# Kernel optimization log

Measured on AMD Instinct MI355X. Metric: run time of the kernel, lower is better.

## Reference

```python
import jax, jax.numpy as jnp
import numpy as np

BSZ, L, D = 8, 2048, 1024

def setup_inputs() -> dict:
    key = jax.random.key(0)
    k1, k2, k3, k4 = jax.random.split(key, 4)
    s = 1.0 / np.sqrt(D)
    return {
        "x":   jax.random.normal(k1, (BSZ, L, D), dtype=jnp.float32),
        "A":   jax.random.normal(k2, (D,), dtype=jnp.float32),
        "W_B": jax.random.normal(k3, (D, D), dtype=jnp.float32) * s,
        "b_B": jnp.zeros((D,), dtype=jnp.float32),
        "W_C": jax.random.normal(k4, (D, D), dtype=jnp.float32) * s,
        "b_C": jnp.zeros((D,), dtype=jnp.float32),
    }

def reference(x, A, W_B, b_B, W_C, b_C):
    # Precompute B(x_t) for all t in one GEMM: [B, L, D]
    Bx = jnp.einsum("bld,ed->ble", x, W_B) + b_B
    h0 = jnp.zeros((x.shape[0], x.shape[2]), dtype=x.dtype)

    def step(h, bx_t):
        h = jnp.tanh(A * h + bx_t)   # elementwise recurrence
        return h, h

    # scan over time: Bx -> [L, B, D]
    _, hs = jax.lax.scan(step, h0, jnp.swapaxes(Bx, 0, 1))
    # y_t = C(h_t), batched over all t: hs [L, B, D]
    y = jnp.einsum("lbd,ed->lbe", hs, W_C) + b_C
    return jnp.swapaxes(y, 0, 1)  # [B, L, D]
```

## Files before the change

### kernel.cpp

```cpp
#include <hip/hip_runtime.h>
#include <hip/hip_bf16.h>
#include <stdint.h>


using half8 = __attribute__((ext_vector_type(8))) _Float16;
using f32x4 = __attribute__((ext_vector_type(4))) float;

#define DEV __device__ __forceinline__

#if __has_builtin(__builtin_amdgcn_exp2f)
DEV float pexp(float x) { return __builtin_amdgcn_exp2f(x); }
constexpr float BX_SCALE = 2.8853900817779268f;
#else
DEV float pexp(float x) { return __expf(x); }
constexpr float BX_SCALE = 2.0f;
#endif

DEV ushort f2h(float x) {
  union { _Float16 f; ushort u; } c;
  c.f = (_Float16)x;
  return c.u;
}
DEV float h2f(ushort u) {
  union { ushort u; _Float16 f; } c;
  c.u = u;
  return (float)c.f;
}

DEV void gload_lds16(const void* g, void* l) {
  __builtin_amdgcn_global_load_lds((const __attribute__((address_space(1))) void*)g,
                                   (__attribute__((address_space(3))) void*)l,
                                   16, 0, 0);
}

__global__ void k_split_convert(const float* __restrict__ in, ushort* __restrict__ hi,
                                ushort* __restrict__ lo, int n4) {
  const int stride = gridDim.x * blockDim.x;
  for (int i = blockIdx.x * blockDim.x + threadIdx.x; i < n4; i += stride) {
    float4 v = reinterpret_cast<const float4*>(in)[i];
    ushort4 hv, lv;
    hv.x = f2h(v.x); lv.x = f2h(v.x - h2f(hv.x));
    hv.y = f2h(v.y); lv.y = f2h(v.y - h2f(hv.y));
    hv.z = f2h(v.z); lv.z = f2h(v.z - h2f(hv.z));
    hv.w = f2h(v.w); lv.w = f2h(v.w - h2f(hv.w));
    reinterpret_cast<ushort4*>(hi)[i] = hv;
    reinterpret_cast<ushort4*>(lo)[i] = lv;
  }
}

__global__ void k_convert(const float* __restrict__ in, ushort* __restrict__ out, int n4) {
  const int stride = gridDim.x * blockDim.x;
  for (int i = blockIdx.x * blockDim.x + threadIdx.x; i < n4; i += stride) {
    float4 v = reinterpret_cast<const float4*>(in)[i];
    ushort4 hv;
    hv.x = f2h(v.x); hv.y = f2h(v.y);
    hv.z = f2h(v.z); hv.w = f2h(v.w);
    reinterpret_cast<ushort4*>(out)[i] = hv;
  }
}

template <int SPLIT, int SCALE>
__global__ __launch_bounds__(256, 2)
void k_gemm_bt(const ushort* __restrict__ Ah, const ushort* __restrict__ Al,
               const ushort* __restrict__ Bh, const ushort* __restrict__ Bl,
               const float* __restrict__ bias, float* __restrict__ C,
               int M, int N, int K) {
  constexpr int NMAT = SPLIT ? 4 : 2;
  __shared__ __align__(1024) ushort lds[NMAT * 128 * 64];
  ushort* sAh = lds;
  ushort* sAl = lds + (SPLIT ? 8192 : 0);
  ushort* sBh = lds + (SPLIT ? 16384 : 8192);
  ushort* sBl = lds + (SPLIT ? 24576 : 8192);

  const int t = threadIdx.x;
  const int lane = t & 63;
  const int w = t >> 6;
  const int wm = w >> 1, wn = w & 1;

  int bm, bn;
  if (gridDim.x == 8) {
    const int l = blockIdx.y * 8 + blockIdx.x;
    const int xcd = l & 7, s = l >> 3;
    bm = ((s >> 3) << 3) | xcd;
    bn = s & 7;
  } else {
    bm = blockIdx.y; bn = blockIdx.x;
  }

  const int lr = lane & 15;
  const int lk = (lane >> 4) << 3;

  const ushort* gA_h = Ah + (size_t)(bm * 128) * K;
  const ushort* gA_l = SPLIT ? (Al + (size_t)(bm * 128) * K) : gA_h;
  const ushort* gB_h = Bh + (size_t)(bn * 128) * K;
  const ushort* gB_l = SPLIT ? (Bl + (size_t)(bn * 128) * K) : gB_h;

  f32x4 acc[4][4];
#pragma unroll
  for (int i = 0; i < 4; ++i)
#pragma unroll
    for (int j = 0; j < 4; ++j)
#pragma unroll
      for (int r = 0; r < 4; ++r) acc[i][j][r] = 0.f;

  auto stage = [&](int kt) {
    const int k0 = kt * 64;
#pragma unroll
    for (int i = 0; i < 4; ++i) {
      const int lin16 = i * 256 + t;
      const int lb = lin16 << 4;
      const int row = lb >> 7;
      const int srcb = (lb & 127) ^ ((row & 7) << 4);
      const size_t goff = (size_t)row * K + (size_t)(k0 + (srcb >> 1));
      const int lidx = i * 2048 + w * 512;
      gload_lds16(gA_h + goff, sAh + lidx);
      if (SPLIT) gload_lds16(gA_l + goff, sAl + lidx);
      gload_lds16(gB_h + goff, sBh + lidx);
      if (SPLIT) gload_lds16(gB_l + goff, sBl + lidx);
    }
  };

  auto ldfrag = [&](const ushort* s, int row, int kc) -> half8 {
    const int byte = (row << 7) + (((kc << 1) ^ ((row & 7) << 4)));
    return *reinterpret_cast<const half8*>(reinterpret_cast<const char*>(s) + byte);
  };

  const int NT = K / 64;
  stage(0);
  for (int kt = 0; kt < NT; ++kt) {
    __syncthreads();
#pragma unroll
    for (int kk = 0; kk < 2; ++kk) {
      half8 ah[4], bh[4], al[4], bl[4];
      const int kc = kk * 32 + lk;
#pragma unroll
      for (int i = 0; i < 4; ++i) {
        const int row = wm * 64 + i * 16 + lr;
        ah[i] = ldfrag(sAh, row, kc);
        if (SPLIT) al[i] = ldfrag(sAl, row, kc);
      }
#pragma unroll
      for (int j = 0; j < 4; ++j) {
        const int row = wn * 64 + j * 16 + lr;
        bh[j] = ldfrag(sBh, row, kc);
        if (SPLIT) bl[j] = ldfrag(sBl, row, kc);
      }
#pragma unroll
      for (int i = 0; i < 4; ++i)
#pragma unroll
        for (int j = 0; j < 4; ++j) {
          acc[i][j] = __builtin_amdgcn_mfma_f32_16x16x32_f16(ah[i], bh[j], acc[i][j], 0, 0, 0);
          if (SPLIT) {
            acc[i][j] = __builtin_amdgcn_mfma_f32_16x16x32_f16(al[i], bh[j], acc[i][j], 0, 0, 0);
            acc[i][j] = __builtin_amdgcn_mfma_f32_16x16x32_f16(ah[i], bl[j], acc[i][j], 0, 0, 0);
          }
        }
    }
    __syncthreads();
    if (kt + 1 < NT) stage(kt + 1);
  }

  float* Cb = C + (size_t)(bm * 128) * N + bn * 128;
#pragma unroll
  for (int i = 0; i < 4; ++i)
#pragma unroll
    for (int j = 0; j < 4; ++j) {
      const int col = wn * 64 + j * 16 + lr;
      const float bv = bias[bn * 128 + col];
#pragma unroll
      for (int r = 0; r < 4; ++r) {
        const int rowt = wm * 64 + i * 16 + ((lane >> 4) << 2) + r;
        float o = acc[i][j][r] + bv;
        if (SCALE) o *= BX_SCALE;
        Cb[(size_t)rowt * N + col] = o;
      }
    }
}

__global__ __launch_bounds__(64)
void k_recurrence(const float* __restrict__ Bx2, const float* __restrict__ Avec,
                  ushort* __restrict__ Hout) {
  const int tid = blockIdx.x * 64 + threadIdx.x;
  const int b = tid >> 10;
  const int d = tid & 1023;
  const float a2 = BX_SCALE * Avec[d];
  const float* bx = Bx2 + (size_t)b * 2048 * 1024 + d;
  ushort* ho = Hout + (size_t)b * 2048 * 1024 + d;

  constexpr int P = 32;
  constexpr int NC = 2048 / P;
  float bufA[P], bufB[P];
#pragma unroll
  for (int i = 0; i < P; ++i) bufA[i] = bx[(size_t)i * 1024];
#pragma unroll
  for (int i = 0; i < P; ++i) bufB[i] = bx[(size_t)(P + i) * 1024];

  float h = 0.f;
  for (int c = 0; c < NC; c += 2) {
#pragma unroll
    for (int i = 0; i < P; ++i) {
      const float u2 = fmaf(a2, h, bufA[i]);
      const float p  = pexp(u2);
      const float r  = __builtin_amdgcn_rcpf(p + 1.f);
      h = fmaf(-2.f, r, 1.f);
      ho[(size_t)(c * P + i) * 1024] = f2h(h);
    }
    if (c + 2 < NC) {
#pragma unroll
      for (int i = 0; i < P; ++i) bufA[i] = bx[(size_t)((c + 2) * P + i) * 1024];
    }
#pragma unroll
    for (int i = 0; i < P; ++i) {
      const float u2 = fmaf(a2, h, bufB[i]);
      const float p  = pexp(u2);
      const float r  = __builtin_amdgcn_rcpf(p + 1.f);
      h = fmaf(-2.f, r, 1.f);
      ho[(size_t)((c + 1) * P + i) * 1024] = f2h(h);
    }
    if (c + 3 < NC) {
#pragma unroll
      for (int i = 0; i < P; ++i) bufB[i] = bx[(size_t)((c + 3) * P + i) * 1024];
    }
  }
}

extern "C" void kernel_launch(void* const* d_in, const int* in_sizes, int n_in,
                              void* d_out, int out_size, void* d_ws, size_t ws_size,
                              hipStream_t stream) {
  const float* x   = (const float*)d_in[0];
  const float* A   = (const float*)d_in[1];
  const float* W_B = (const float*)d_in[2];
  const float* b_B = (const float*)d_in[3];
  const float* W_C = (const float*)d_in[4];
  const float* b_C = (const float*)d_in[5];
  float* y = (float*)d_out;

  const int Bsz = 8, L = 2048, D = 1024;
  const int M = Bsz * L;

  char* ws = (char*)d_ws;
  ushort* x_hi  = (ushort*)(ws);
  ushort* x_lo  = (ushort*)(ws + 33554432);
  ushort* wb_hi = (ushort*)(ws + 67108864);
  ushort* wb_lo = (ushort*)(ws + 69206016);
  ushort* wc    = (ushort*)(ws + 71303168);
  float*  Bx    = (float*)(ws + 73400320);
  ushort* h     = x_hi;

  k_split_convert<<<2048, 256, 0, stream>>>(x, x_hi, x_lo, M * D / 4);
  k_split_convert<<<512, 256, 0, stream>>>(W_B, wb_hi, wb_lo, D * D / 4);
  k_convert<<<512, 256, 0, stream>>>(W_C, wc, D * D / 4);

  k_gemm_bt<1, 1><<<dim3(D / 128, M / 128), 256, 0, stream>>>(
      x_hi, x_lo, wb_hi, wb_lo, b_B, Bx, M, D, D);

  k_recurrence<<<(Bsz * D) / 64, 64, 0, stream>>>(Bx, A, h);

  k_gemm_bt<0, 0><<<dim3(D / 128, M / 128), 256, 0, stream>>>(
      h, (const ushort*)nullptr, wc, (const ushort*)nullptr, b_C, y, M, D, D);
}
```

Before: 232.6 us.

## Double-buffer GEMM LDS with BK=32, fuse weight conversions, simplify recurrence math

The GEMM now uses two LDS buffers with a 32-wide K step and a new swizzle. It prefetches two stages ahead and waits with explicit vmcnt counts, so global-to-LDS loads overlap MFMA work. It also raises launch bounds to allow more occupancy for the non-split GEMM. The two weight-conversion kernels are merged into one launch, and the tanh recurrence is rewritten in terms of the sigmoid reciprocal, which removes one FMA from the serial dependency chain. The hand-tuned waitcnt values and the new swizzle risk subtle hazards or bank conflicts.

```diff
diff --git a/kernel.cpp b/kernel.cpp
--- a/kernel.cpp
+++ b/kernel.cpp
@@ -48,29 +48,39 @@
   }
 }
 
-__global__ void k_convert(const float* __restrict__ in, ushort* __restrict__ out, int n4) {
+__global__ void k_convert_weights(const float* __restrict__ WB, const float* __restrict__ WC,
+                                  ushort* __restrict__ wbh, ushort* __restrict__ wbl,
+                                  ushort* __restrict__ wch, int n4) {
   const int stride = gridDim.x * blockDim.x;
-  for (int i = blockIdx.x * blockDim.x + threadIdx.x; i < n4; i += stride) {
-    float4 v = reinterpret_cast<const float4*>(in)[i];
-    ushort4 hv;
-    hv.x = f2h(v.x); hv.y = f2h(v.y);
-    hv.z = f2h(v.z); hv.w = f2h(v.w);
-    reinterpret_cast<ushort4*>(out)[i] = hv;
+  for (int i = blockIdx.x * blockDim.x + threadIdx.x; i < 2 * n4; i += stride) {
+    if (i < n4) {
+      float4 v = reinterpret_cast<const float4*>(WB)[i];
+      ushort4 hv, lv;
+      hv.x = f2h(v.x); lv.x = f2h(v.x - h2f(hv.x));
+      hv.y = f2h(v.y); lv.y = f2h(v.y - h2f(hv.y));
+      hv.z = f2h(v.z); lv.z = f2h(v.z - h2f(hv.z));
+      hv.w = f2h(v.w); lv.w = f2h(v.w - h2f(hv.w));
+      reinterpret_cast<ushort4*>(wbh)[i] = hv;
+      reinterpret_cast<ushort4*>(wbl)[i] = lv;
+    } else {
+      const int j = i - n4;
+      float4 v = reinterpret_cast<const float4*>(WC)[j];
+      ushort4 hv;
+      hv.x = f2h(v.x); hv.y = f2h(v.y);
+      hv.z = f2h(v.z); hv.w = f2h(v.w);
+      reinterpret_cast<ushort4*>(wch)[j] = hv;
+    }
   }
 }
 
 template <int SPLIT, int SCALE>
-__global__ __launch_bounds__(256, 2)
+__global__ __launch_bounds__(256, SPLIT ? 2 : 4)
 void k_gemm_bt(const ushort* __restrict__ Ah, const ushort* __restrict__ Al,
                const ushort* __restrict__ Bh, const ushort* __restrict__ Bl,
                const float* __restrict__ bias, float* __restrict__ C,
                int M, int N, int K) {
   constexpr int NMAT = SPLIT ? 4 : 2;
-  __shared__ __align__(1024) ushort lds[NMAT * 128 * 64];
-  ushort* sAh = lds;
-  ushort* sAl = lds + (SPLIT ? 8192 : 0);
-  ushort* sBh = lds + (SPLIT ? 16384 : 8192);
-  ushort* sBl = lds + (SPLIT ? 24576 : 8192);
+  __shared__ __align__(1024) ushort lds[2 * NMAT * 4096];
 
   const int t = threadIdx.x;
   const int lane = t & 63;
@@ -78,17 +88,15 @@
   const int wm = w >> 1, wn = w & 1;
 
   int bm, bn;
-  if (gridDim.x == 8) {
+  {
     const int l = blockIdx.y * 8 + blockIdx.x;
     const int xcd = l & 7, s = l >> 3;
     bm = ((s >> 3) << 3) | xcd;
     bn = s & 7;
-  } else {
-    bm = blockIdx.y; bn = blockIdx.x;
   }
 
   const int lr = lane & 15;
-  const int lk = (lane >> 4) << 3;
+  const int kcb = (lane >> 4) << 4;
 
   const ushort* gA_h = Ah + (size_t)(bm * 128) * K;
   const ushort* gA_l = SPLIT ? (Al + (size_t)(bm * 128) * K) : gA_h;
@@ -103,62 +111,81 @@
 #pragma unroll
       for (int r = 0; r < 4; ++r) acc[i][j][r] = 0.f;
 
-  auto stage = [&](int kt) {
-    const int k0 = kt * 64;
+  auto stage = [&](int kt, int buf) {
+    const int k0 = kt * 32;
+    ushort* base = lds + buf * (NMAT * 4096);
+#pragma unroll
+    for (int i = 0; i < 2; ++i) {
+      const int lin16 = i * 256 + t;
+      const int line = lin16 >> 3;
+      const int row = (line << 1) | ((lin16 >> 2) & 1);
+      const int kb = ((lin16 & 3) << 4) ^ ((line & 3) << 4);
+      const size_t goff = (size_t)row * K + (size_t)(k0 + (kb >> 1));
+      const int dst = lin16 << 3;
+      gload_lds16(gA_h + goff, base + dst);
+      gload_lds16(gB_h + goff, base + (SPLIT ? 2 : 1) * 4096 + dst);
+      if (SPLIT) {
+        gload_lds16(gA_l + goff, base + 4096 + dst);
+        gload_lds16(gB_l + goff, base + 3 * 4096 + dst);
+      }
+    }
+  };
+
+  auto ldfrag = [&](const ushort* mat, int row) -> half8 {
+    const int line = row >> 1;
+    const int off = (line << 7) + ((row & 1) << 6) + (kcb ^ ((line & 3) << 4));
+    return *reinterpret_cast<const half8*>(reinterpret_cast<const char*>(mat) + off);
+  };
+
+  const int NT = K / 32;
+  stage(0, 0);
+  stage(1, 1);
+
+  auto kstep = [&](int kt, bool last) {
+    if (last)        asm volatile("s_waitcnt vmcnt(0)" ::: "memory");
+    else if (SPLIT)  asm volatile("s_waitcnt vmcnt(8)" ::: "memory");
+    else             asm volatile("s_waitcnt vmcnt(4)" ::: "memory");
+    __builtin_amdgcn_sched_barrier(0);
+    __builtin_amdgcn_s_barrier();
+    __builtin_amdgcn_sched_barrier(0);
+
+    const ushort* base = lds + (kt & 1) * (NMAT * 4096);
+    const ushort* sAh = base;
+    const ushort* sAl = base + 4096;
+    const ushort* sBh = base + (SPLIT ? 2 : 1) * 4096;
+    const ushort* sBl = base + 3 * 4096;
+
+    half8 ah[4], al[4], bh[4], bl[4];
 #pragma unroll
     for (int i = 0; i < 4; ++i) {
-      const int lin16 = i * 256 + t;
-      const int lb = lin16 << 4;
-      const int row = lb >> 7;
-      const int srcb = (lb & 127) ^ ((row & 7) << 4);
-      const size_t goff = (size_t)row * K + (size_t)(k0 + (srcb >> 1));
-      const int lidx = i * 2048 + w * 512;
-      gload_lds16(gA_h + goff, sAh + lidx);
-      if (SPLIT) gload_lds16(gA_l + goff, sAl + lidx);
-      gload_lds16(gB_h + goff, sBh + lidx);
-      if (SPLIT) gload_lds16(gB_l + goff, sBl + lidx);
-    }
+      const int r = wm * 64 + i * 16 + lr;
+      ah[i] = ldfrag(sAh, r);
+      if (SPLIT) al[i] = ldfrag(sAl, r);
+    }
+#pragma unroll
+    for (int j = 0; j < 4; ++j) {
+      const int r = wn * 64 + j * 16 + lr;
+      bh[j] = ldfrag(sBh, r);
+      if (SPLIT) bl[j] = ldfrag(sBl, r);
+    }
+#pragma unroll
+    for (int i = 0; i < 4; ++i)
+#pragma unroll
+      for (int j = 0; j < 4; ++j) {
+        acc[i][j] = __builtin_amdgcn_mfma_f32_16x16x32_f16(ah[i], bh[j], acc[i][j], 0, 0, 0);
+        if (SPLIT) {
+          acc[i][j] = __builtin_amdgcn_mfma_f32_16x16x32_f16(al[i], bh[j], acc[i][j], 0, 0, 0);
+          acc[i][j] = __builtin_amdgcn_mfma_f32_16x16x32_f16(ah[i], bl[j], acc[i][j], 0, 0, 0);
+        }
+      }
+
+    __builtin_amdgcn_sched_barrier(0);
+    __builtin_amdgcn_s_barrier();
+    if (kt + 2 < NT) stage(kt + 2, kt & 1);
   };
 
-  auto ldfrag = [&](const ushort* s, int row, int kc) -> half8 {
-    const int byte = (row << 7) + (((kc << 1) ^ ((row & 7) << 4)));
-    return *reinterpret_cast<const half8*>(reinterpret_cast<const char*>(s) + byte);
-  };
-
-  const int NT = K / 64;
-  stage(0);
-  for (int kt = 0; kt < NT; ++kt) {
-    __syncthreads();
-#pragma unroll
-    for (int kk = 0; kk < 2; ++kk) {
-      half8 ah[4], bh[4], al[4], bl[4];
-      const int kc = kk * 32 + lk;
-#pragma unroll
-      for (int i = 0; i < 4; ++i) {
-        const int row = wm * 64 + i * 16 + lr;
-        ah[i] = ldfrag(sAh, row, kc);
-        if (SPLIT) al[i] = ldfrag(sAl, row, kc);
-      }
-#pragma unroll
-      for (int j = 0; j < 4; ++j) {
-        const int row = wn * 64 + j * 16 + lr;
-        bh[j] = ldfrag(sBh, row, kc);
-        if (SPLIT) bl[j] = ldfrag(sBl, row, kc);
-      }
-#pragma unroll
-      for (int i = 0; i < 4; ++i)
-#pragma unroll
-        for (int j = 0; j < 4; ++j) {
-          acc[i][j] = __builtin_amdgcn_mfma_f32_16x16x32_f16(ah[i], bh[j], acc[i][j], 0, 0, 0);
-          if (SPLIT) {
-            acc[i][j] = __builtin_amdgcn_mfma_f32_16x16x32_f16(al[i], bh[j], acc[i][j], 0, 0, 0);
-            acc[i][j] = __builtin_amdgcn_mfma_f32_16x16x32_f16(ah[i], bl[j], acc[i][j], 0, 0, 0);
-          }
-        }
-    }
-    __syncthreads();
-    if (kt + 1 < NT) stage(kt + 1);
-  }
+  for (int kt = 0; kt < NT - 1; ++kt) kstep(kt, false);
+  kstep(NT - 1, true);
 
   float* Cb = C + (size_t)(bm * 128) * N + bn * 128;
 #pragma unroll
@@ -184,42 +211,39 @@
   const int b = tid >> 10;
   const int d = tid & 1023;
   const float a2 = BX_SCALE * Avec[d];
+  const float na2 = -2.f * a2;
   const float* bx = Bx2 + (size_t)b * 2048 * 1024 + d;
   ushort* ho = Hout + (size_t)b * 2048 * 1024 + d;
 
   constexpr int P = 32;
   constexpr int NC = 2048 / P;
-  float bufA[P], bufB[P];
-#pragma unroll
-  for (int i = 0; i < P; ++i) bufA[i] = bx[(size_t)i * 1024];
-#pragma unroll
-  for (int i = 0; i < P; ++i) bufB[i] = bx[(size_t)(P + i) * 1024];
-
-  float h = 0.f;
+  float cA[P], cB[P];
+#pragma unroll
+  for (int i = 0; i < P; ++i) cA[i] = a2 + bx[(size_t)i * 1024];
+#pragma unroll
+  for (int i = 0; i < P; ++i) cB[i] = a2 + bx[(size_t)(P + i) * 1024];
+
+  float r = 0.5f;
   for (int c = 0; c < NC; c += 2) {
 #pragma unroll
     for (int i = 0; i < P; ++i) {
-      const float u2 = fmaf(a2, h, bufA[i]);
-      const float p  = pexp(u2);
-      const float r  = __builtin_amdgcn_rcpf(p + 1.f);
-      h = fmaf(-2.f, r, 1.f);
-      ho[(size_t)(c * P + i) * 1024] = f2h(h);
+      const float u2 = fmaf(na2, r, cA[i]);
+      r = __builtin_amdgcn_rcpf(pexp(u2) + 1.f);
+      ho[(size_t)(c * P + i) * 1024] = f2h(fmaf(-2.f, r, 1.f));
     }
     if (c + 2 < NC) {
 #pragma unroll
-      for (int i = 0; i < P; ++i) bufA[i] = bx[(size_t)((c + 2) * P + i) * 1024];
+      for (int i = 0; i < P; ++i) cA[i] = a2 + bx[(size_t)((c + 2) * P + i) * 1024];
     }
 #pragma unroll
     for (int i = 0; i < P; ++i) {
-      const float u2 = fmaf(a2, h, bufB[i]);
-      const float p  = pexp(u2);
-      const float r  = __builtin_amdgcn_rcpf(p + 1.f);
-      h = fmaf(-2.f, r, 1.f);
-      ho[(size_t)((c + 1) * P + i) * 1024] = f2h(h);
+      const float u2 = fmaf(na2, r, cB[i]);
+      r = __builtin_amdgcn_rcpf(pexp(u2) + 1.f);
+      ho[(size_t)((c + 1) * P + i) * 1024] = f2h(fmaf(-2.f, r, 1.f));
     }
     if (c + 3 < NC) {
 #pragma unroll
-      for (int i = 0; i < P; ++i) bufB[i] = bx[(size_t)((c + 3) * P + i) * 1024];
+      for (int i = 0; i < P; ++i) cB[i] = a2 + bx[(size_t)((c + 3) * P + i) * 1024];
     }
   }
 }
@@ -239,23 +263,22 @@
   const int M = Bsz * L;
 
   char* ws = (char*)d_ws;
-  ushort* x_hi  = (ushort*)(ws);
-  ushort* x_lo  = (ushort*)(ws + 33554432);
-  ushort* wb_hi = (ushort*)(ws + 67108864);
-  ushort* wb_lo = (ushort*)(ws + 69206016);
-  ushort* wc    = (ushort*)(ws + 71303168);
-  float*  Bx    = (float*)(ws + 73400320);
-  ushort* h     = x_hi;
+  ushort* x_hi = (ushort*)(ws);
+  ushort* x_lo = (ushort*)(ws + 33554432);
+  ushort* wbh  = (ushort*)(ws + 67108864);
+  ushort* wbl  = (ushort*)(ws + 69206016);
+  ushort* wch  = (ushort*)(ws + 71303168);
+  float*  Bx   = (float*)(ws + 73400320);
+  ushort* h    = x_hi;
 
   k_split_convert<<<2048, 256, 0, stream>>>(x, x_hi, x_lo, M * D / 4);
-  k_split_convert<<<512, 256, 0, stream>>>(W_B, wb_hi, wb_lo, D * D / 4);
-  k_convert<<<512, 256, 0, stream>>>(W_C, wc, D * D / 4);
-
-  k_gemm_bt<1, 1><<<dim3(D / 128, M / 128), 256, 0, stream>>>(
-      x_hi, x_lo, wb_hi, wb_lo, b_B, Bx, M, D, D);
+  k_convert_weights<<<512, 256, 0, stream>>>(W_B, W_C, wbh, wbl, wch, D * D / 4);
+
+  k_gemm_bt<1, 1><<<dim3(8, M / 128), 256, 0, stream>>>(
+      x_hi, x_lo, wbh, wbl, b_B, Bx, M, D, D);
 
   k_recurrence<<<(Bsz * D) / 64, 64, 0, stream>>>(Bx, A, h);
 
-  k_gemm_bt<0, 0><<<dim3(D / 128, M / 128), 256, 0, stream>>>(
-      h, (const ushort*)nullptr, wc, (const ushort*)nullptr, b_C, y, M, D, D);
-}
+  k_gemm_bt<0, 0><<<dim3(8, M / 128), 256, 0, stream>>>(
+      h, (const ushort*)nullptr, wch, (const ushort*)nullptr, b_C, y, M, D, D);
+}
```

Result: slower. 262.5 us (+12.8%).
